# Kernel tuning notes

Hardware: AMD Instinct MI355X
Metric: run time of the kernel (lower is better)

## Reference

```python
import jax, jax.numpy as jnp
import numpy as np

A = 2048        # atoms
IN_DEPTH = 128
OUT_DEPTH = 128
FILTER_LEN = 16


def setup_inputs() -> dict:
    key = jax.random.key(0)
    k1, k2, k3, k4 = jax.random.split(key, 4)
    node_property_tensor = jax.random.normal(k1, (A, IN_DEPTH), dtype=jnp.float32)
    connectivity_tensor = jax.random.normal(k2, (A, A, FILTER_LEN), dtype=jnp.float32)
    bond_property_tensor = jax.random.normal(k3, (A, FILTER_LEN, 2), dtype=jnp.float32)
    # filters initialized ~ N(0,1) * 1/in_depth, per the torch init
    filters = jax.random.normal(k4, (OUT_DEPTH, FILTER_LEN, IN_DEPTH + 2), dtype=jnp.float32) / IN_DEPTH
    return {
        "node_property_tensor": node_property_tensor,
        "connectivity_tensor": connectivity_tensor,
        "bond_property_tensor": bond_property_tensor,
        "filters": filters,
    }


def reference(node_property_tensor, connectivity_tensor, bond_property_tensor, filters):
    # gather neighbor features: conn (A,B,F) x node (B,D) -> (A,F,D)
    node_connection = jnp.einsum('abf,bd->afd', connectivity_tensor, node_property_tensor)
    # append bond properties -> (A, F, D+2)
    combined = jnp.concatenate([node_connection, bond_property_tensor], axis=2)
    # fused broadcast-multiply + double-sum: (A,F,K) x (O,F,K) -> (A,O)
    return jnp.einsum('afk,ofk->ao', combined, filters)
```

## Files before the change

### kernel.cpp

```cpp
#include <hip/hip_runtime.h>
#include <stdint.h>

#define N_ATOM 2048
#define K_TOT  32768
#define KCH    2048
#define BK2    128
#define NIT    (KCH / BK2)
#define NPART  16

typedef __attribute__((ext_vector_type(8))) short bf16x8;
typedef __attribute__((ext_vector_type(4))) float f32x4;

typedef __attribute__((address_space(3))) uint32_t lds_u32;
typedef __attribute__((address_space(1))) uint32_t gbl_u32;

__device__ __forceinline__ void async_ld16(const void* g, void* l) {
  __builtin_amdgcn_global_load_lds((const gbl_u32*)g, (lds_u32*)l, 16, 0, 0);
}

__device__ __forceinline__ unsigned short f2bf(float x) {
  union { float f; uint32_t u; } v; v.f = x;
  uint32_t r = v.u + 0x7FFFu + ((v.u >> 16) & 1u);
  return (unsigned short)(r >> 16);
}

__device__ __forceinline__ uint32_t pack_bf2(float x, float y) {
  union { float f; uint32_t u; } a, b;
  a.f = x; b.f = y;
  uint32_t au = a.u + 0x7FFFu;
  uint32_t bu = b.u + 0x7FFFu;
  return __builtin_amdgcn_perm(bu, au, 0x07060302u);
}

__global__ __launch_bounds__(256) void k_gt(const float* __restrict__ node,
                                            const float* __restrict__ filt,
                                            unsigned short* __restrict__ Gt) {
  __shared__ unsigned short As[128 * 136];
  __shared__ unsigned short Bs[128 * 136];
  const int t  = threadIdx.x;
  const int b0 = blockIdx.x * 128;
  const int n0 = blockIdx.y * 128;

#pragma unroll
  for (int rep = 0; rep < 16; ++rep) {
    int q = rep * 256 + t;
    int row = q >> 5, c4 = q & 31;
    float4 v = *(const float4*)(node + (size_t)(b0 + row) * 128 + c4 * 4);
    unsigned short* dst = &As[row * 136 + c4 * 4];
    dst[0] = f2bf(v.x); dst[1] = f2bf(v.y); dst[2] = f2bf(v.z); dst[3] = f2bf(v.w);
  }
#pragma unroll
  for (int rep = 0; rep < 32; ++rep) {
    int q = rep * 256 + t;
    int row = q >> 6, c2 = q & 63;
    float2 v = *(const float2*)(filt + (size_t)(n0 + row) * 130 + c2 * 2);
    unsigned short* dst = &Bs[row * 136 + c2 * 2];
    dst[0] = f2bf(v.x); dst[1] = f2bf(v.y);
  }
  __syncthreads();

  const int w = t >> 6, l = t & 63;
  const int lm = l & 15, q4 = l >> 4;

  f32x4 acc[2][8];
#pragma unroll
  for (int ms = 0; ms < 2; ++ms)
#pragma unroll
    for (int ns = 0; ns < 8; ++ns)
      acc[ms][ns] = (f32x4){0.f, 0.f, 0.f, 0.f};

#pragma unroll
  for (int ks = 0; ks < 4; ++ks) {
    int ko = ks * 32 + q4 * 8;
    bf16x8 a[2], b[8];
#pragma unroll
    for (int ms = 0; ms < 2; ++ms) {
      int m = w * 32 + ms * 16 + lm;
      a[ms] = *(const bf16x8*)&As[m * 136 + ko];
    }
#pragma unroll
    for (int ns = 0; ns < 8; ++ns) {
      int n = ns * 16 + lm;
      b[ns] = *(const bf16x8*)&Bs[n * 136 + ko];
    }
#pragma unroll
    for (int ms = 0; ms < 2; ++ms)
#pragma unroll
      for (int ns = 0; ns < 8; ++ns)
        acc[ms][ns] = __builtin_amdgcn_mfma_f32_16x16x32_bf16(a[ms], b[ns], acc[ms][ns], 0, 0, 0);
  }

#pragma unroll
  for (int ms = 0; ms < 2; ++ms)
#pragma unroll
    for (int ns = 0; ns < 8; ++ns)
#pragma unroll
      for (int i = 0; i < 4; ++i) {
        int m = w * 32 + ms * 16 + q4 * 4 + i;
        int n = ns * 16 + lm;
        Gt[(size_t)(b0 + m) * 2048 + n0 + n] = f2bf(acc[ms][ns][i]);
      }
}

__global__ __launch_bounds__(256) void k_bond(const float* __restrict__ bond,
                                              const float* __restrict__ filt,
                                              float* __restrict__ out) {
  __shared__ float fb[128 * 32];
  __shared__ float bl[16 * 32];
  const int t  = threadIdx.x;
  const int a0 = blockIdx.x * 16;

#pragma unroll
  for (int r = 0; r < 16; ++r) {
    int idx = r * 256 + t;
    int o = idx >> 5, fj = idx & 31;
    int f = fj >> 1, j = fj & 1;
    fb[idx] = filt[(size_t)o * 2080 + f * 130 + 128 + j];
  }
  bl[t]       = bond[(size_t)a0 * 32 + t];
  bl[256 + t] = bond[(size_t)a0 * 32 + 256 + t];
  __syncthreads();

#pragma unroll
  for (int r = 0; r < 8; ++r) {
    int idx = r * 256 + t;
    int aa = idx >> 7, o = idx & 127;
    const float2* bp = (const float2*)&bl[aa * 32];
    const float2* fp = (const float2*)&fb[o * 32];
    float acc = 0.f;
#pragma unroll
    for (int f = 0; f < 16; ++f) {
      float2 b2 = bp[f], f2 = fp[f];
      acc += b2.x * f2.x + b2.y * f2.y;
    }
    out[(size_t)(a0 + aa) * 128 + o] = acc;
  }
}

__global__ __launch_bounds__(512, 2) void k_main(const float* __restrict__ conn,
                                                 const unsigned short* __restrict__ Gt,
                                                 float* __restrict__ P) {
  __shared__ unsigned short Bh[2][8 * 128 * 16];

  const int t  = threadIdx.x;
  const int w  = t >> 6, l = t & 63;
  const int lm = l & 15, q4 = l >> 4;
  const int a0 = blockIdx.x * 128;
  const int kc = blockIdx.y * KCH;

  f32x4 acc[8];
#pragma unroll
  for (int ns = 0; ns < 8; ++ns)
    acc[ns] = (f32x4){0.f, 0.f, 0.f, 0.f};

  const float* arow = conn + (size_t)(a0 + w * 16 + lm) * K_TOT;

  auto stageB = [&](int buf, int k0) {
    const char* gB = (const char*)(Gt + (size_t)k0 * 128);
#pragma unroll
    for (int r = 0; r < 4; ++r) {
      const void* g = gB + (size_t)(r * 512 + t) * 16;
      void* lb = (void*)((char*)&Bh[buf][0] + r * 8192 + w * 1024);
      async_ld16(g, lb);
    }
  };

  f32x4 Ar[4][2];
  auto loadA = [&](int k0) {
#pragma unroll
    for (int kk = 0; kk < 4; ++kk) {
      const float* p = arow + k0 + kk * 32 + q4 * 8;
      Ar[kk][0] = *(const f32x4*)p;
      Ar[kk][1] = *(const f32x4*)(p + 4);
    }
  };

  stageB(0, kc);
  loadA(kc);
  __syncthreads();

  for (int it = 0; it < NIT; ++it) {
    const int cur = it & 1;

    bf16x8 af[4];
#pragma unroll
    for (int kk = 0; kk < 4; ++kk) {
      f32x4 lo = Ar[kk][0], hi = Ar[kk][1];
      union { bf16x8 v; uint32_t u[4]; } cvt;
      cvt.u[0] = pack_bf2(lo[0], lo[1]);
      cvt.u[1] = pack_bf2(lo[2], lo[3]);
      cvt.u[2] = pack_bf2(hi[0], hi[1]);
      cvt.u[3] = pack_bf2(hi[2], hi[3]);
      af[kk] = cvt.v;
    }

    if (it + 1 < NIT) {
      stageB(1 - cur, kc + (it + 1) * BK2);
      loadA(kc + (it + 1) * BK2);
    }

#pragma unroll
    for (int kk = 0; kk < 4; ++kk) {
      const int b_rel = 2 * kk + (q4 >> 1);
      const int f0 = (q4 & 1) * 8;
#pragma unroll
      for (int ns = 0; ns < 8; ++ns) {
        int o = ns * 16 + lm;
        bf16x8 b = *(const bf16x8*)&Bh[cur][b_rel * 2048 + o * 16 + f0];
        acc[ns] = __builtin_amdgcn_mfma_f32_16x16x32_bf16(af[kk], b, acc[ns], 0, 0, 0);
      }
    }

    __syncthreads();
  }

  float* Pt = P + (size_t)blockIdx.y * (N_ATOM * 128);
#pragma unroll
  for (int ns = 0; ns < 8; ++ns)
#pragma unroll
    for (int i = 0; i < 4; ++i) {
      int m = w * 16 + q4 * 4 + i;
      int n = ns * 16 + lm;
      Pt[(size_t)(a0 + m) * 128 + n] = acc[ns][i];
    }
}

__global__ __launch_bounds__(256) void k_red(const float* __restrict__ P,
                                             float* __restrict__ out) {
  const int idx = blockIdx.x * 256 + threadIdx.x;
  f32x4 s = *(const f32x4*)(out + (size_t)idx * 4);
#pragma unroll
  for (int c = 0; c < NPART; ++c) {
    f32x4 p = *(const f32x4*)(P + (size_t)c * (N_ATOM * 128) + (size_t)idx * 4);
    s[0] += p[0]; s[1] += p[1]; s[2] += p[2]; s[3] += p[3];
  }
  *(f32x4*)(out + (size_t)idx * 4) = s;
}

extern "C" void kernel_launch(void* const* d_in, const int* in_sizes, int n_in,
                              void* d_out, int out_size, void* d_ws, size_t ws_size,
                              hipStream_t stream) {
  const float* node = (const float*)d_in[0];
  const float* conn = (const float*)d_in[1];
  const float* bond = (const float*)d_in[2];
  const float* filt = (const float*)d_in[3];
  float* out = (float*)d_out;

  const size_t gt_bytes = (size_t)N_ATOM * 2048 * sizeof(unsigned short);
  const size_t p_bytes  = (size_t)NPART * N_ATOM * 128 * sizeof(float);
  if (ws_size < gt_bytes + p_bytes) return;

  unsigned short* Gt = (unsigned short*)d_ws;
  float* P = (float*)((char*)d_ws + gt_bytes);

  k_gt  <<<dim3(16, 16), 256, 0, stream>>>(node, filt, Gt);
  k_bond<<<dim3(128),    256, 0, stream>>>(bond, filt, out);
  k_main<<<dim3(16, 16), 512, 0, stream>>>(conn, Gt, P);
  k_red <<<dim3(256),    256, 0, stream>>>(P, out);
}
```

Baseline: 434.0 us.

## Read filter tile directly from global, drop LDS staging, double per-wave rows

The main GEMM kernel no longer stages the Gt tile through LDS with async loads and barriers. Each wave now loads B fragments straight from global/L2 and computes 32 atom rows instead of 16, reusing each B fragment across two MFMAs. The split-K is doubled to 32 partitions with 256-thread blocks, and streaming conn loads are marked nontemporal. The goal is to remove the LDS traffic and barrier stalls, at the cost of more global/L2 reads of Gt and a larger partial-sum buffer to reduce.

```diff
diff --git a/kernel.cpp b/kernel.cpp
--- a/kernel.cpp
+++ b/kernel.cpp
@@ -3,20 +3,13 @@
 
 #define N_ATOM 2048
 #define K_TOT  32768
-#define KCH    2048
+#define KCH    1024
 #define BK2    128
 #define NIT    (KCH / BK2)
-#define NPART  16
+#define NPART  32
 
 typedef __attribute__((ext_vector_type(8))) short bf16x8;
 typedef __attribute__((ext_vector_type(4))) float f32x4;
-
-typedef __attribute__((address_space(3))) uint32_t lds_u32;
-typedef __attribute__((address_space(1))) uint32_t gbl_u32;
-
-__device__ __forceinline__ void async_ld16(const void* g, void* l) {
-  __builtin_amdgcn_global_load_lds((const gbl_u32*)g, (lds_u32*)l, 16, 0, 0);
-}
 
 __device__ __forceinline__ unsigned short f2bf(float x) {
   union { float f; uint32_t u; } v; v.f = x;
@@ -137,92 +130,87 @@
   }
 }
 
-__global__ __launch_bounds__(512, 2) void k_main(const float* __restrict__ conn,
+__global__ __launch_bounds__(256, 2) void k_main(const float* __restrict__ conn,
                                                  const unsigned short* __restrict__ Gt,
                                                  float* __restrict__ P) {
-  __shared__ unsigned short Bh[2][8 * 128 * 16];
-
   const int t  = threadIdx.x;
   const int w  = t >> 6, l = t & 63;
   const int lm = l & 15, q4 = l >> 4;
-  const int a0 = blockIdx.x * 128;
-  const int kc = blockIdx.y * KCH;
-
-  f32x4 acc[8];
-#pragma unroll
-  for (int ns = 0; ns < 8; ++ns)
-    acc[ns] = (f32x4){0.f, 0.f, 0.f, 0.f};
-
-  const float* arow = conn + (size_t)(a0 + w * 16 + lm) * K_TOT;
-
-  auto stageB = [&](int buf, int k0) {
-    const char* gB = (const char*)(Gt + (size_t)k0 * 128);
-#pragma unroll
-    for (int r = 0; r < 4; ++r) {
-      const void* g = gB + (size_t)(r * 512 + t) * 16;
-      void* lb = (void*)((char*)&Bh[buf][0] + r * 8192 + w * 1024);
-      async_ld16(g, lb);
+  const int kc = blockIdx.x * KCH;
+  const int ab = blockIdx.y * 128 + w * 32;
+
+  f32x4 acc[2][8];
+#pragma unroll
+  for (int ms = 0; ms < 2; ++ms)
+#pragma unroll
+    for (int ns = 0; ns < 8; ++ns)
+      acc[ms][ns] = (f32x4){0.f, 0.f, 0.f, 0.f};
+
+  const float* arow0 = conn + (size_t)(ab + lm) * K_TOT;
+  const float* arow1 = conn + (size_t)(ab + 16 + lm) * K_TOT;
+
+  f32x4 Ar[2][4][2];
+  auto loadA = [&](int k0) {
+#pragma unroll
+    for (int kk = 0; kk < 4; ++kk) {
+      const float* p0 = arow0 + k0 + kk * 32 + q4 * 8;
+      const float* p1 = arow1 + k0 + kk * 32 + q4 * 8;
+      Ar[0][kk][0] = __builtin_nontemporal_load((const f32x4*)p0);
+      Ar[0][kk][1] = __builtin_nontemporal_load((const f32x4*)(p0 + 4));
+      Ar[1][kk][0] = __builtin_nontemporal_load((const f32x4*)p1);
+      Ar[1][kk][1] = __builtin_nontemporal_load((const f32x4*)(p1 + 4));
     }
   };
 
-  f32x4 Ar[4][2];
-  auto loadA = [&](int k0) {
+  const int f0 = (q4 & 1) * 8;
+  const int bq = q4 >> 1;
+
+  loadA(kc);
+
+  for (int it = 0; it < NIT; ++it) {
+    bf16x8 af[2][4];
+#pragma unroll
+    for (int ms = 0; ms < 2; ++ms)
+#pragma unroll
+      for (int kk = 0; kk < 4; ++kk) {
+        f32x4 lo = Ar[ms][kk][0], hi = Ar[ms][kk][1];
+        union { bf16x8 v; uint32_t u[4]; } cvt;
+        cvt.u[0] = pack_bf2(lo[0], lo[1]);
+        cvt.u[1] = pack_bf2(lo[2], lo[3]);
+        cvt.u[2] = pack_bf2(hi[0], hi[1]);
+        cvt.u[3] = pack_bf2(hi[2], hi[3]);
+        af[ms][kk] = cvt.v;
+      }
+
+    if (it + 1 < NIT) loadA(kc + (it + 1) * BK2);
+
+    const int kb_base = (kc + it * BK2) >> 4;
 #pragma unroll
     for (int kk = 0; kk < 4; ++kk) {
-      const float* p = arow + k0 + kk * 32 + q4 * 8;
-      Ar[kk][0] = *(const f32x4*)p;
-      Ar[kk][1] = *(const f32x4*)(p + 4);
-    }
-  };
-
-  stageB(0, kc);
-  loadA(kc);
-  __syncthreads();
-
-  for (int it = 0; it < NIT; ++it) {
-    const int cur = it & 1;
-
-    bf16x8 af[4];
-#pragma unroll
-    for (int kk = 0; kk < 4; ++kk) {
-      f32x4 lo = Ar[kk][0], hi = Ar[kk][1];
-      union { bf16x8 v; uint32_t u[4]; } cvt;
-      cvt.u[0] = pack_bf2(lo[0], lo[1]);
-      cvt.u[1] = pack_bf2(lo[2], lo[3]);
-      cvt.u[2] = pack_bf2(hi[0], hi[1]);
-      cvt.u[3] = pack_bf2(hi[2], hi[3]);
-      af[kk] = cvt.v;
-    }
-
-    if (it + 1 < NIT) {
-      stageB(1 - cur, kc + (it + 1) * BK2);
-      loadA(kc + (it + 1) * BK2);
-    }
-
-#pragma unroll
-    for (int kk = 0; kk < 4; ++kk) {
-      const int b_rel = 2 * kk + (q4 >> 1);
-      const int f0 = (q4 & 1) * 8;
+      const unsigned short* gb = Gt + (size_t)(kb_base + 2 * kk + bq) * 2048 + f0;
+      bf16x8 b[8];
+#pragma unroll
+      for (int ns = 0; ns < 8; ++ns)
+        b[ns] = *(const bf16x8*)(gb + (ns * 16 + lm) * 16);
 #pragma unroll
       for (int ns = 0; ns < 8; ++ns) {
-        int o = ns * 16 + lm;
-        bf16x8 b = *(const bf16x8*)&Bh[cur][b_rel * 2048 + o * 16 + f0];
-        acc[ns] = __builtin_amdgcn_mfma_f32_16x16x32_bf16(af[kk], b, acc[ns], 0, 0, 0);
-      }
-    }
-
-    __syncthreads();
-  }
-
-  float* Pt = P + (size_t)blockIdx.y * (N_ATOM * 128);
-#pragma unroll
-  for (int ns = 0; ns < 8; ++ns)
-#pragma unroll
-    for (int i = 0; i < 4; ++i) {
-      int m = w * 16 + q4 * 4 + i;
-      int n = ns * 16 + lm;
-      Pt[(size_t)(a0 + m) * 128 + n] = acc[ns][i];
-    }
+        acc[0][ns] = __builtin_amdgcn_mfma_f32_16x16x32_bf16(af[0][kk], b[ns], acc[0][ns], 0, 0, 0);
+        acc[1][ns] = __builtin_amdgcn_mfma_f32_16x16x32_bf16(af[1][kk], b[ns], acc[1][ns], 0, 0, 0);
+      }
+    }
+  }
+
+  float* Pt = P + (size_t)blockIdx.x * (N_ATOM * 128);
+#pragma unroll
+  for (int ms = 0; ms < 2; ++ms)
+#pragma unroll
+    for (int ns = 0; ns < 8; ++ns)
+#pragma unroll
+      for (int i = 0; i < 4; ++i) {
+        int m = ab + ms * 16 + q4 * 4 + i;
+        int n = ns * 16 + lm;
+        Pt[(size_t)m * 128 + n] = acc[ms][ns][i];
+      }
 }
 
 __global__ __launch_bounds__(256) void k_red(const float* __restrict__ P,
@@ -255,6 +243,6 @@
 
   k_gt  <<<dim3(16, 16), 256, 0, stream>>>(node, filt, Gt);
   k_bond<<<dim3(128),    256, 0, stream>>>(bond, filt, out);
-  k_main<<<dim3(16, 16), 512, 0, stream>>>(conn, Gt, P);
+  k_main<<<dim3(32, 16), 256, 0, stream>>>(conn, Gt, P);
   k_red <<<dim3(256),    256, 0, stream>>>(P, out);
 }
```

New measurement: 437.4 us. No clear change (+0.8%).
